# Kernel optimization log

Measured on AMD Instinct MI355X. Metric: run time of the kernel, lower is better.

## Reference

```python
import jax, jax.numpy as jnp
import numpy as np

INF = jnp.float32(jnp.inf)
# 8 grid directions (the torch module always uses all 8; self.diagonal is never read)
DIRS = jnp.array([[-1, 0], [1, 0], [0, -1], [0, 1],
                  [-1, -1], [-1, 1], [1, -1], [1, 1]], dtype=jnp.int32)


def setup_inputs() -> dict:
    key = jax.random.key(0)
    b, n = 128, 32
    weights = jax.random.uniform(key, (b, n, n), dtype=jnp.float32)
    return {"weights": weights}


def _dijkstra_path(weights):
    b, n, _ = weights.shape
    ar = jnp.arange(b)

    dist = jnp.full((b, n, n), INF, dtype=weights.dtype).at[:, 0, 0].set(0.0)
    vis = jnp.zeros((b, n, n), dtype=bool)
    pred = jnp.zeros((b, n, n, 2), dtype=jnp.int32)

    def relax_step(_, state):
        dist, vis, pred = state
        # pick unvisited node with minimum distance, per batch element
        unvis = jnp.where(vis, INF, dist)                       # (b, n, n)
        idx = jnp.argmin(unvis.reshape(b, -1), axis=1)          # (b,)
        cy, cx = idx // n, idx % n
        vis = vis.at[ar, cy, cx].set(True)
        cur = dist[ar, cy, cx]                                   # (b,)

        # 8 neighbors, vectorized over the direction axis
        ny = cy[:, None] + DIRS[None, :, 0]                      # (b, 8)
        nx = cx[:, None] + DIRS[None, :, 1]
        valid = (ny >= 0) & (ny < n) & (nx >= 0) & (nx < n)
        nyc = jnp.clip(ny, 0, n - 1)
        nxc = jnp.clip(nx, 0, n - 1)
        bb = jnp.broadcast_to(ar[:, None], (b, 8))

        old = dist[bb, nyc, nxc]
        nvis = vis[bb, nyc, nxc]
        new = cur[:, None] + weights[bb, nyc, nxc]
        upd = valid & ~nvis & (new < old)

        # duplicate-safe relaxation: scatter-min with inf where no update
        dist = dist.at[bb, nyc, nxc].min(jnp.where(upd, new, INF))
        # cells updated this step all get predecessor (cy, cx)
        umask = jnp.zeros((b, n, n), dtype=bool).at[bb, nyc, nxc].max(upd)
        cur_yx = jnp.stack([cy, cx], axis=-1)[:, None, None, :]  # (b,1,1,2)
        pred = jnp.where(umask[..., None], cur_yx.astype(pred.dtype), pred)
        return dist, vis, pred

    # Running the full n*n relaxations is equivalent to the torch early-break:
    # by Dijkstra's invariant, the target's distance/predecessor are final once
    # it would be popped, and later pops never alter the target path.
    dist, vis, pred = jax.lax.fori_loop(0, n * n, relax_step, (dist, vis, pred))

    # backtrack from (n-1, n-1) to (0, 0); pred[0,0] == (0,0) so it is a fixed point
    path = jnp.zeros((b, n, n), dtype=jnp.float32).at[:, n - 1, n - 1].set(1.0)

    def back_step(_, state):
        path, cy, cx = state
        py = pred[ar, cy, cx, 0]
        px = pred[ar, cy, cx, 1]
        path = path.at[ar, py, px].set(1.0)
        return path, py, px

    start = jnp.full((b,), n - 1, dtype=jnp.int32)
    path, _, _ = jax.lax.fori_loop(0, n * n, back_step, (path, start, start))
    return path


def reference(weights) -> jnp.ndarray:
    return _dijkstra_path(weights)
```

## Files before the change

### kernel.cpp

```cpp
#include <hip/hip_runtime.h>

#define N  32
#define NN (N * N)

__global__ __launch_bounds__(NN, 1) void dijkstra_path_kernel(
    const float* __restrict__ weights, float* __restrict__ out)
{
    const int b = blockIdx.x;
    const int t = threadIdx.x;
    const int y = t >> 5;
    const int x = t & 31;

    __shared__ float dist[NN];
    __shared__ int   pred[NN];
    __shared__ unsigned char pathm[NN];

    const float INF = __builtin_huge_valf();
    const float wme = weights[b * NN + t];

    dist[t]  = (t == 0) ? 0.0f : INF;
    pathm[t] = 0;

    const int dyv[8] = {-1, 1, 0, 0, -1, -1, 1, 1};
    const int dxv[8] = { 0, 0,-1, 1, -1,  1,-1, 1};
    int nbr[8];
    unsigned validm = 0;
    #pragma unroll
    for (int k = 0; k < 8; ++k) {
        int ny = y + dyv[k], nx = x + dxv[k];
        bool ok = (ny >= 0) && (ny < N) && (nx >= 0) && (nx < N);
        nbr[k] = ok ? (ny * N + nx) : t;
        if (ok) validm |= (1u << k);
    }
    __syncthreads();

    for (int it = 0; it < 4096; ++it) {
        float old = dist[t];
        float v = old;
        #pragma unroll
        for (int k = 0; k < 8; ++k)
            v = fminf(v, dist[nbr[k]] + wme);
        int changed = (v < old) ? 1 : 0;
        if (changed) dist[t] = v;
        if (__syncthreads_or(changed) == 0) break;
    }

    int p = 0;
    if (t != 0) {
        float best = INF;
        #pragma unroll
        for (int k = 0; k < 8; ++k) {
            if (validm & (1u << k)) {
                float c = dist[nbr[k]] + wme;
                if (c < best) { best = c; p = nbr[k]; }
            }
        }
    }
    pred[t] = p;
    __syncthreads();

    if (t == 0) {
        int cur = NN - 1;
        pathm[cur] = 1;
        for (int s = 0; s < NN && cur != 0; ++s) {
            cur = pred[cur];
            pathm[cur] = 1;
        }
    }
    __syncthreads();

    out[b * NN + t] = pathm[t] ? 1.0f : 0.0f;
}

extern "C" void kernel_launch(void* const* d_in, const int* in_sizes, int n_in,
                              void* d_out, int out_size, void* d_ws, size_t ws_size,
                              hipStream_t stream) {
    const float* w = (const float*)d_in[0];
    float* out = (float*)d_out;
    const int b = in_sizes[0] / NN;
    dijkstra_path_kernel<<<dim3(b), dim3(NN), 0, stream>>>(w, out);
}
```

Measured before the change: 84.28 us.

## Use single-wavefront blocks with register-tiled 4x4 Bellman-Ford sweeps

Replaces the 1024-thread-per-batch Jacobi relaxation with one 64-lane wavefront per batch, where each lane holds a 4x4 tile plus halo in registers. It runs forward and backward Gauss-Seidel sweeps within each tile per iteration, so distances propagate further per step. The block-wide barrier becomes a wave-level any-vote over a padded shared grid. It also vectorizes the output stores. The aim is fewer iterations and cheaper synchronization, at the cost of far fewer threads per block and lower occupancy per batch.

```diff
diff --git a/kernel.cpp b/kernel.cpp
--- a/kernel.cpp
+++ b/kernel.cpp
@@ -1,75 +1,138 @@
 #include <hip/hip_runtime.h>
 
-#define N  32
-#define NN (N * N)
+#define N   32
+#define NN  1024
+#define PS  34
+#define PSZ (PS * PS)
 
-__global__ __launch_bounds__(NN, 1) void dijkstra_path_kernel(
+__global__ __launch_bounds__(64, 1) void dijkstra_path_kernel(
     const float* __restrict__ weights, float* __restrict__ out)
 {
-    const int b = blockIdx.x;
-    const int t = threadIdx.x;
-    const int y = t >> 5;
-    const int x = t & 31;
+    const int b    = blockIdx.x;
+    const int lane = threadIdx.x;
+    const int ty   = lane >> 3;
+    const int tx   = lane & 7;
+    const int y0   = ty << 2;
+    const int x0   = tx << 2;
 
-    __shared__ float dist[NN];
+    __shared__ float dist[PSZ];
     __shared__ int   pred[NN];
-    __shared__ unsigned char pathm[NN];
+    __shared__ float pathf[NN];
 
     const float INF = __builtin_huge_valf();
-    const float wme = weights[b * NN + t];
 
-    dist[t]  = (t == 0) ? 0.0f : INF;
-    pathm[t] = 0;
+    #pragma unroll
+    for (int k = 0; k < 19; ++k) {
+        int idx = lane + k * 64;
+        if (idx < PSZ) dist[idx] = INF;
+    }
+    #pragma unroll
+    for (int k = 0; k < 16; ++k) pathf[lane + k * 64] = 0.0f;
 
-    const int dyv[8] = {-1, 1, 0, 0, -1, -1, 1, 1};
-    const int dxv[8] = { 0, 0,-1, 1, -1,  1,-1, 1};
-    int nbr[8];
-    unsigned validm = 0;
+    float w[4][4];
+    const float* wb = weights + b * NN;
     #pragma unroll
-    for (int k = 0; k < 8; ++k) {
-        int ny = y + dyv[k], nx = x + dxv[k];
-        bool ok = (ny >= 0) && (ny < N) && (nx >= 0) && (nx < N);
-        nbr[k] = ok ? (ny * N + nx) : t;
-        if (ok) validm |= (1u << k);
+    for (int i = 0; i < 4; ++i) {
+        const float4 v = *(const float4*)(wb + (y0 + i) * N + x0);
+        w[i][0] = v.x; w[i][1] = v.y; w[i][2] = v.z; w[i][3] = v.w;
+    }
+
+    float g[6][6];
+    #pragma unroll
+    for (int i = 0; i < 6; ++i)
+        #pragma unroll
+        for (int j = 0; j < 6; ++j) g[i][j] = INF;
+    if (lane == 0) {
+        g[1][1] = 0.0f;
+        dist[1 * PS + 1] = 0.0f;
     }
     __syncthreads();
 
-    for (int it = 0; it < 4096; ++it) {
-        float old = dist[t];
-        float v = old;
+    const int base_top = y0 * PS + x0;
+    const int base_bot = (y0 + 5) * PS + x0;
+    for (int it = 0; it < 512; ++it) {
         #pragma unroll
-        for (int k = 0; k < 8; ++k)
-            v = fminf(v, dist[nbr[k]] + wme);
-        int changed = (v < old) ? 1 : 0;
-        if (changed) dist[t] = v;
-        if (__syncthreads_or(changed) == 0) break;
+        for (int j = 0; j < 6; ++j) g[0][j] = dist[base_top + j];
+        #pragma unroll
+        for (int j = 0; j < 6; ++j) g[5][j] = dist[base_bot + j];
+        #pragma unroll
+        for (int i = 0; i < 4; ++i) {
+            g[1 + i][0] = dist[(y0 + i + 1) * PS + x0];
+            g[1 + i][5] = dist[(y0 + i + 1) * PS + x0 + 5];
+        }
+
+        bool changed = false;
+        #pragma unroll
+        for (int i = 1; i <= 4; ++i)
+            #pragma unroll
+            for (int j = 1; j <= 4; ++j) {
+                float m = fminf(
+                    fminf(fminf(g[i-1][j-1], g[i-1][j]), fminf(g[i-1][j+1], g[i][j-1])),
+                    fminf(fminf(g[i][j+1], g[i+1][j-1]), fminf(g[i+1][j], g[i+1][j+1])));
+                float nv = m + w[i-1][j-1];
+                if (nv < g[i][j]) { g[i][j] = nv; changed = true; }
+            }
+        #pragma unroll
+        for (int i = 4; i >= 1; --i)
+            #pragma unroll
+            for (int j = 4; j >= 1; --j) {
+                float m = fminf(
+                    fminf(fminf(g[i-1][j-1], g[i-1][j]), fminf(g[i-1][j+1], g[i][j-1])),
+                    fminf(fminf(g[i][j+1], g[i+1][j-1]), fminf(g[i+1][j], g[i+1][j+1])));
+                float nv = m + w[i-1][j-1];
+                if (nv < g[i][j]) { g[i][j] = nv; changed = true; }
+            }
+
+        if (changed) {
+            #pragma unroll
+            for (int i = 0; i < 4; ++i)
+                #pragma unroll
+                for (int j = 0; j < 4; ++j)
+                    dist[(y0 + i + 1) * PS + (x0 + j + 1)] = g[1 + i][1 + j];
+        }
+        __syncthreads();
+        if (!__any((int)changed)) break;
     }
 
-    int p = 0;
-    if (t != 0) {
-        float best = INF;
+    const int dy[8] = {-1, 1, 0, 0, -1, -1, 1, 1};
+    const int dx[8] = { 0, 0,-1, 1, -1,  1,-1, 1};
+    #pragma unroll
+    for (int i = 0; i < 4; ++i)
         #pragma unroll
-        for (int k = 0; k < 8; ++k) {
-            if (validm & (1u << k)) {
-                float c = dist[nbr[k]] + wme;
-                if (c < best) { best = c; p = nbr[k]; }
+        for (int j = 0; j < 4; ++j) {
+            const int yy = y0 + i, xx = x0 + j;
+            const int t  = yy * N + xx;
+            int p = 0;
+            if (t != 0) {
+                float best = INF;
+                #pragma unroll
+                for (int k = 0; k < 8; ++k) {
+                    float u = g[1 + i + dy[k]][1 + j + dx[k]];
+                    float c = u + w[i][j];
+                    if (c < best) { best = c; p = (yy + dy[k]) * N + (xx + dx[k]); }
+                }
             }
+            pred[t] = p;
         }
-    }
-    pred[t] = p;
     __syncthreads();
 
-    if (t == 0) {
+    if (lane == 0) {
         int cur = NN - 1;
-        pathm[cur] = 1;
+        pathf[cur] = 1.0f;
         for (int s = 0; s < NN && cur != 0; ++s) {
             cur = pred[cur];
-            pathm[cur] = 1;
+            pathf[cur] = 1.0f;
         }
     }
     __syncthreads();
 
-    out[b * NN + t] = pathm[t] ? 1.0f : 0.0f;
+    float* ob = out + b * NN;
+    #pragma unroll
+    for (int i = 0; i < 4; ++i) {
+        const int t = (y0 + i) * N + x0;
+        float4 v = *(float4*)&pathf[t];
+        *(float4*)(ob + t) = v;
+    }
 }
 
 extern "C" void kernel_launch(void* const* d_in, const int* in_sizes, int n_in,
@@ -78,5 +141,5 @@
     const float* w = (const float*)d_in[0];
     float* out = (float*)d_out;
     const int b = in_sizes[0] / NN;
-    dijkstra_path_kernel<<<dim3(b), dim3(NN), 0, stream>>>(w, out);
+    dijkstra_path_kernel<<<dim3(b), dim3(64), 0, stream>>>(w, out);
 }
```

Result: faster. 74.43 us (-11.7%).
